# Kernel tuning notes

Measured on AMD Instinct MI355X. Metric: run time of the kernel, lower is better.

Reference implementation:

```python
import jax, jax.numpy as jnp
import numpy as np

D_MODEL = 512
N_HEADS = 8
D_HEAD = D_MODEL // N_HEADS
D_FF = 2048
L_Q = 22          # forecast_horizon
FACTOR = 5        # prob_sparse_factor
EPS = 1e-5


def positional_encoding(L, d):
    pos = jnp.arange(L, dtype=jnp.float32)[:, None]
    div = jnp.exp(-jnp.arange(0, d, 2, dtype=jnp.float32) * (np.log(10000.0) / d))
    pe = jnp.zeros((L, d), dtype=jnp.float32)
    pe = pe.at[:, 0::2].set(jnp.sin(pos * div))
    pe = pe.at[:, 1::2].set(jnp.cos(pos * div))
    return pe


def layernorm(x, g, b):
    mu = x.mean(-1, keepdims=True)
    var = ((x - mu) ** 2).mean(-1, keepdims=True)
    return (x - mu) * jax.lax.rsqrt(var + EPS) * g + b


def setup_inputs() -> dict:
    key = jax.random.key(0)
    ks = jax.random.split(key, 8)
    s = 0.02
    return {
        "encoder_output": jax.random.normal(ks[0], (32, 4096, D_MODEL), dtype=jnp.float32),
        "Wq": jax.random.normal(ks[1], (D_MODEL, D_MODEL), dtype=jnp.float32) * s,
        "bq": jnp.zeros((D_MODEL,), jnp.float32),
        "Wk": jax.random.normal(ks[2], (D_MODEL, D_MODEL), dtype=jnp.float32) * s,
        "bk": jnp.zeros((D_MODEL,), jnp.float32),
        "Wv": jax.random.normal(ks[3], (D_MODEL, D_MODEL), dtype=jnp.float32) * s,
        "bv": jnp.zeros((D_MODEL,), jnp.float32),
        "Wo": jax.random.normal(ks[4], (D_MODEL, D_MODEL), dtype=jnp.float32) * s,
        "bo": jnp.zeros((D_MODEL,), jnp.float32),
        "conv1_w": jax.random.normal(ks[5], (D_FF, D_MODEL), dtype=jnp.float32) * s,  # Conv1d k=1
        "conv1_b": jnp.zeros((D_FF,), jnp.float32),
        "conv2_w": jax.random.normal(ks[6], (D_MODEL, D_FF), dtype=jnp.float32) * s,
        "conv2_b": jnp.zeros((D_MODEL,), jnp.float32),
        "gamma1": jnp.ones((D_MODEL,), jnp.float32),
        "beta1": jnp.zeros((D_MODEL,), jnp.float32),
        "gamma2": jnp.ones((D_MODEL,), jnp.float32),
        "beta2": jnp.zeros((D_MODEL,), jnp.float32),
        "Wout": jax.random.normal(ks[7], (D_MODEL, 1), dtype=jnp.float32) * s,
        "bout": jnp.zeros((1,), jnp.float32),
    }


def reference(encoder_output, Wq, bq, Wk, bk, Wv, bv, Wo, bo,
              conv1_w, conv1_b, conv2_w, conv2_b,
              gamma1, beta1, gamma2, beta2, Wout, bout):
    B, L_K, _ = encoder_output.shape
    # queries are pure positional encodings of a zero dummy input
    pe = positional_encoding(L_Q, D_MODEL)[None]                      # [1, L_Q, d]
    q = (pe @ Wq + bq).reshape(1, L_Q, N_HEADS, D_HEAD).transpose(0, 2, 1, 3)
    k = (encoder_output @ Wk + bk).reshape(B, L_K, N_HEADS, D_HEAD).transpose(0, 2, 1, 3)
    v = (encoder_output @ Wv + bv).reshape(B, L_K, N_HEADS, D_HEAD).transpose(0, 2, 1, 3)

    # --- deterministic ProbSparse query selection (Informer-style) ---
    sample_k = min(L_K, FACTOR * int(np.ceil(np.log(L_K))))           # 45
    n_top = min(L_Q, FACTOR * int(np.ceil(np.log(L_Q))))              # 20
    k_idx = (jnp.arange(sample_k) * L_K) // sample_k                  # deterministic strided key sample
    k_samp = k[:, :, k_idx]                                           # [B,h,sk,dh]
    qk_s = jnp.einsum('ahqd,bhkd->bhqk', q, k_samp)                   # [B,h,L_Q,sk]
    M = qk_s.max(-1) - qk_s.mean(-1)                                  # sparsity measure [B,h,L_Q]
    _, top_idx = jax.lax.top_k(M, n_top)                              # [B,h,n_top]

    q_b = jnp.broadcast_to(q, (B, N_HEADS, L_Q, D_HEAD))
    q_top = jnp.take_along_axis(q_b, top_idx[..., None], axis=2)      # [B,h,n_top,dh]
    scale = 1.0 / np.sqrt(D_HEAD)
    attn = jax.nn.softmax(jnp.einsum('bhud,bhkd->bhuk', q_top, k) * scale, axis=-1)
    ctx_top = jnp.einsum('bhuk,bhkd->bhud', attn, v)                  # [B,h,n_top,dh]

    # non-selected queries get mean(V) (no causal mask: cross attention)
    ctx = jnp.broadcast_to(v.mean(axis=2, keepdims=True), (B, N_HEADS, L_Q, D_HEAD))
    b_i = jnp.arange(B)[:, None, None]
    h_i = jnp.arange(N_HEADS)[None, :, None]
    ctx = ctx.at[b_i, h_i, top_idx].set(ctx_top)

    attn_out = ctx.transpose(0, 2, 1, 3).reshape(B, L_Q, D_MODEL) @ Wo + bo

    # eval-mode dropout is identity -> norm1(attn + dropout(attn)) == norm1(2*attn)
    x = layernorm(attn_out + attn_out, gamma1, beta1)
    ff = jax.nn.relu(x @ conv1_w.T + conv1_b)                          # conv1d k=1 == pointwise linear
    ff = ff @ conv2_w.T + conv2_b
    y = layernorm(x + ff, gamma2, beta2)                               # [B,L_Q,d]
    forecasts = (y @ Wout + bout).squeeze(-1)                          # [B,L_Q]
    return forecasts, y
```

## Files before the change

### kernel.cpp

```cpp
#include <hip/hip_runtime.h>
#include <math.h>

#define B_ 32
#define LK 4096
#define C_ 512
#define H_ 8
#define DH 64
#define U_ 22
#define HU 176
#define HUP 192
#define SK 45
#define NTOP 20
#define DFF 2048
#define EPSF 1e-5f

typedef unsigned short u16;
typedef __attribute__((ext_vector_type(8))) short short8;
typedef __attribute__((ext_vector_type(4))) short short4v;
typedef __attribute__((ext_vector_type(8))) unsigned short ushort8;
typedef __attribute__((ext_vector_type(4))) unsigned short ushort4v;
typedef __attribute__((ext_vector_type(4))) float f32x4;

__device__ __forceinline__ u16 f2b(float f){
  union{float f;unsigned u;} v; v.f=f;
  unsigned r=(v.u + 0x7FFFu + ((v.u>>16)&1u))>>16;
  return (u16)r;
}
__device__ __forceinline__ float b2f(u16 h){
  union{unsigned u;float f;} v; v.u=((unsigned)h)<<16; return v.f;
}
__device__ __forceinline__ short8 ldfrag(const u16* p){
  short4v lo=*(const short4v*)p;
  short4v hi=*(const short4v*)(p+16);
  short8 r;
  r[0]=lo[0];r[1]=lo[1];r[2]=lo[2];r[3]=lo[3];
  r[4]=hi[0];r[5]=hi[1];r[6]=hi[2];r[7]=hi[3];
  return r;
}
__device__ __forceinline__ float blocksum(float v, float* red){
  for(int off=32;off;off>>=1) v+=__shfl_xor(v,off);
  int w=threadIdx.x>>6, lane=threadIdx.x&63;
  if(lane==0) red[w]=v;
  __syncthreads();
  float r=red[0]+red[1]+red[2]+red[3];
  __syncthreads();
  return r;
}

__global__ void k_prep_q(const float* __restrict__ Wq, const float* __restrict__ bq,
                         float* __restrict__ q){
  __shared__ float pe[C_];
  int u=blockIdx.x, t=threadIdx.x;
  float lg = logf(10000.0f)/(float)C_;
  for(int c=t;c<C_;c+=256){
    int i=c>>1;
    float arg=(float)u*expf(-(float)(2*i)*lg);
    pe[c]=(c&1)?cosf(arg):sinf(arg);
  }
  __syncthreads();
  for(int col=t;col<C_;col+=256){
    float acc=0.f;
    for(int c=0;c<C_;c++) acc+=pe[c]*Wq[c*C_+col];
    q[u*C_+col]=acc+bq[col];
  }
}

__global__ void k_qeff(const float* __restrict__ q, const float* __restrict__ Wk,
                       float* __restrict__ qef, u16* __restrict__ qeb){
  int hu=blockIdx.x, t=threadIdx.x;
  int h=hu/U_, u=hu-h*U_;
  __shared__ float qr[DH];
  bool valid=(hu<HU);
  if(t<DH) qr[t]=valid? q[u*C_+h*DH+t] : 0.f;
  __syncthreads();
  for(int c=t;c<C_;c+=256){
    float acc=0.f;
    if(valid){
      const float* wrow=Wk+(size_t)c*C_+h*DH;
      for(int d=0;d<DH;d++) acc+=qr[d]*wrow[d];
    }
    qef[hu*C_+c]=acc;
    qeb[hu*C_+c]=f2b(acc);
  }
}

__global__ void k_sample(const float* __restrict__ enc, const float* __restrict__ qef,
                         unsigned* __restrict__ selmask){
  int bh=blockIdx.x, t=threadIdx.x;
  int b=bh>>3, h=bh&7;
  __shared__ float es[SK][132];
  __shared__ float qe[U_][132];
  __shared__ float qk[U_][SK+3];
  __shared__ float Mv[U_];
  float acc[4]={0.f,0.f,0.f,0.f};
  for(int c0=0;c0<C_;c0+=128){
    __syncthreads();
    for(int i=t;i<SK*128;i+=256){
      int ks=i>>7, c=i&127;
      int row=(ks*LK)/SK;
      es[ks][c]=enc[((size_t)b*LK+row)*C_+c0+c];
    }
    for(int i=t;i<U_*128;i+=256){
      int u=i>>7, c=i&127;
      qe[u][c]=qef[(h*U_+u)*C_+c0+c];
    }
    __syncthreads();
    for(int dd=0;dd<4;dd++){
      int d=t+dd*256;
      if(d<U_*SK){
        int u=d/SK, ks=d-u*SK;
        float s=0.f;
        for(int c=0;c<128;c++) s+=qe[u][c]*es[ks][c];
        acc[dd]+=s;
      }
    }
  }
  for(int dd=0;dd<4;dd++){
    int d=t+dd*256;
    if(d<U_*SK){ int u=d/SK, ks=d-u*SK; qk[u][ks]=acc[dd]; }
  }
  __syncthreads();
  if(t<U_){
    float mx=-1e30f, sm=0.f;
    for(int ks=0;ks<SK;ks++){ float v=qk[t][ks]; mx=fmaxf(mx,v); sm+=v; }
    Mv[t]=mx-sm/(float)SK;
  }
  __syncthreads();
  if(t<64){
    bool sel=false;
    if(t<U_){
      float m=Mv[t]; int rank=0;
      for(int u2=0;u2<U_;u2++){
        float o=Mv[u2];
        if(o>m || (o==m && u2<t)) rank++;
      }
      sel=(rank<NTOP);
    }
    unsigned long long bal=__ballot(sel);
    if(t==0) selmask[bh]=(unsigned)(bal&0x3FFFFFull);
  }
}

__global__ void k_convert(const float* __restrict__ enc, u16* __restrict__ encb,
                          u16* __restrict__ encT){
  int ct=blockIdx.x, lt=blockIdx.y, b=blockIdx.z, t=threadIdx.x;
  __shared__ __align__(16) u16 tile[64][72];
  int l0=lt*64, c0=ct*64;
  for(int p=0;p<4;p++){
    int lr=p*16+(t>>4);
    int cc=(t&15)*4;
    float4 v=*(const float4*)&enc[((size_t)b*LK+l0+lr)*C_+c0+cc];
    u16 h0=f2b(v.x),h1=f2b(v.y),h2=f2b(v.z),h3=f2b(v.w);
    ushort4v o; o[0]=h0;o[1]=h1;o[2]=h2;o[3]=h3;
    *(ushort4v*)&encb[((size_t)b*LK+l0+lr)*C_+c0+cc]=o;
    tile[cc+0][lr]=h0; tile[cc+1][lr]=h1; tile[cc+2][lr]=h2; tile[cc+3][lr]=h3;
  }
  __syncthreads();
  for(int p=0;p<2;p++){
    int cr=p*32+(t>>3), loff=(t&7)*8;
    ushort8 w=*(const ushort8*)&tile[cr][loff];
    *(ushort8*)&encT[((size_t)b*C_+c0+cr)*LK+l0+loff]=w;
  }
}

__global__ void k_colsum(const u16* __restrict__ encT, float* __restrict__ encsum){
  int b=blockIdx.x;
  int w=threadIdx.x>>6, lane=threadIdx.x&63;
  int c=blockIdx.y*4+w;
  const u16* row=encT+((size_t)b*C_+c)*LK;
  float s=0.f;
  for(int i=0;i<8;i++){
    ushort8 v=*(const ushort8*)&row[(i*64+lane)*8];
    for(int j=0;j<8;j++) s+=b2f(v[j]);
  }
  for(int off=32;off;off>>=1) s+=__shfl_down(s,off);
  if(lane==0) encsum[b*C_+c]=s;
}

__global__ __launch_bounds__(256) void k_scores(const u16* __restrict__ encb,
                                                const u16* __restrict__ qeb,
                                                u16* __restrict__ S){
  int nt=blockIdx.x, b=blockIdx.y, t=threadIdx.x;
  __shared__ __align__(16) u16 qa[HUP][40];
  __shared__ __align__(16) u16 et[128][40];
  int l0=nt*128;
  int w=t>>6, lane=t&63;
  int arow=lane&15, kgrp=(lane>>4)*4;
  f32x4 acc[12][2];
  #pragma unroll
  for(int i=0;i<12;i++){
    acc[i][0]=(f32x4){0.f,0.f,0.f,0.f};
    acc[i][1]=(f32x4){0.f,0.f,0.f,0.f};
  }
  for(int kc=0;kc<C_;kc+=32){
    __syncthreads();
    for(int i=t;i<768;i+=256){
      int r=i>>2, off=(i&3)*8;
      *(ushort8*)&qa[r][off]=*(const ushort8*)&qeb[(size_t)r*C_+kc+off];
    }
    for(int i=t;i<512;i+=256){
      int l=i>>2, off=(i&3)*8;
      *(ushort8*)&et[l][off]=*(const ushort8*)&encb[((size_t)b*LK+l0+l)*C_+kc+off];
    }
    __syncthreads();
    short8 bf0=ldfrag(&et[w*32+arow][kgrp]);
    short8 bf1=ldfrag(&et[w*32+16+arow][kgrp]);
    #pragma unroll
    for(int m=0;m<12;m++){
      short8 af=ldfrag(&qa[m*16+arow][kgrp]);
      acc[m][0]=__builtin_amdgcn_mfma_f32_16x16x32_bf16(af,bf0,acc[m][0],0,0,0);
      acc[m][1]=__builtin_amdgcn_mfma_f32_16x16x32_bf16(af,bf1,acc[m][1],0,0,0);
    }
  }
  int dcol=lane&15, drow=(lane>>4)*4;
  #pragma unroll
  for(int m=0;m<12;m++)
    #pragma unroll
    for(int ns=0;ns<2;ns++){
      size_t base=((size_t)b*HUP+m*16+drow)*LK + l0 + w*32 + ns*16 + dcol;
      #pragma unroll
      for(int r=0;r<4;r++)
        S[base+(size_t)r*LK]=f2b(acc[m][ns][r]);
    }
}

__global__ void k_softmax(u16* __restrict__ S){
  int hu=blockIdx.x, b=blockIdx.y, t=threadIdx.x;
  u16* row=S+((size_t)b*HUP+hu)*LK;
  __shared__ float red[8];
  __shared__ float red2[8];
  float v[16];
  ushort8 r0=*(const ushort8*)&row[t*16];
  ushort8 r1=*(const ushort8*)&row[t*16+8];
  #pragma unroll
  for(int j=0;j<8;j++){ v[j]=b2f(r0[j]); v[8+j]=b2f(r1[j]); }
  float mx=-1e30f;
  #pragma unroll
  for(int j=0;j<16;j++) mx=fmaxf(mx,v[j]);
  for(int off=32;off;off>>=1) mx=fmaxf(mx,__shfl_xor(mx,off));
  int w=t>>6, lane=t&63;
  if(lane==0) red[w]=mx;
  __syncthreads();
  mx=fmaxf(fmaxf(red[0],red[1]),fmaxf(red[2],red[3]));
  const float scale=0.125f;
  float sm=0.f;
  #pragma unroll
  for(int j=0;j<16;j++){ v[j]=__expf((v[j]-mx)*scale); sm+=v[j]; }
  for(int off=32;off;off>>=1) sm+=__shfl_xor(sm,off);
  if(lane==0) red2[w]=sm;
  __syncthreads();
  sm=red2[0]+red2[1]+red2[2]+red2[3];
  float inv=1.f/sm;
  ushort8 o0,o1;
  #pragma unroll
  for(int j=0;j<8;j++){ o0[j]=f2b(v[j]*inv); o1[j]=f2b(v[8+j]*inv); }
  *(ushort8*)&row[t*16]=o0;
  *(ushort8*)&row[t*16+8]=o1;
}

__global__ __launch_bounds__(256) void k_pv(const u16* __restrict__ S,
                                            const u16* __restrict__ encT,
                                            float* __restrict__ ctxA){
  int f=blockIdx.x, t=threadIdx.x;
  int xcd=f&7, s=f>>3;
  int mt=s&3, g=(s>>2)*8+xcd;
  int nt=g>>7, bz=g&127;
  int b=bz>>2, kch=bz&3;
  __shared__ __align__(16) u16 pa[48][72];
  __shared__ __align__(16) u16 et[128][72];
  int hu0=mt*48, c0=nt*128;
  int w=t>>6, lane=t&63;
  int arow=lane&15, kgrp=(lane>>4)*4;
  f32x4 acc[3][2];
  #pragma unroll
  for(int i=0;i<3;i++)
    #pragma unroll
    for(int j=0;j<2;j++) acc[i][j]=(f32x4){0.f,0.f,0.f,0.f};
  int lbase=kch*1024;
  for(int l0=lbase;l0<lbase+1024;l0+=64){
    __syncthreads();
    for(int i=t;i<384;i+=256){
      int r=i>>3, off=(i&7)*8;
      *(ushort8*)&pa[r][off]=*(const ushort8*)&S[((size_t)b*HUP+hu0+r)*LK+l0+off];
    }
    for(int i=t;i<1024;i+=256){
      int r=i>>3, off=(i&7)*8;
      *(ushort8*)&et[r][off]=*(const ushort8*)&encT[((size_t)b*C_+c0+r)*LK+l0+off];
    }
    __syncthreads();
    #pragma unroll
    for(int ks=0;ks<2;ks++){
      short8 af0=ldfrag(&pa[arow][ks*32+kgrp]);
      short8 af1=ldfrag(&pa[16+arow][ks*32+kgrp]);
      short8 af2=ldfrag(&pa[32+arow][ks*32+kgrp]);
      #pragma unroll
      for(int ns=0;ns<2;ns++){
        short8 bf=ldfrag(&et[w*32+ns*16+arow][ks*32+kgrp]);
        acc[0][ns]=__builtin_amdgcn_mfma_f32_16x16x32_bf16(af0,bf,acc[0][ns],0,0,0);
        acc[1][ns]=__builtin_amdgcn_mfma_f32_16x16x32_bf16(af1,bf,acc[1][ns],0,0,0);
        acc[2][ns]=__builtin_amdgcn_mfma_f32_16x16x32_bf16(af2,bf,acc[2][ns],0,0,0);
      }
    }
  }
  int dcol=lane&15, drow=(lane>>4)*4;
  #pragma unroll
  for(int m=0;m<3;m++)
    #pragma unroll
    for(int ns=0;ns<2;ns++)
      #pragma unroll
      for(int r=0;r<4;r++){
        int hu=hu0+m*16+drow+r, c=c0+w*32+ns*16+dcol;
        atomicAdd(&ctxA[((size_t)b*HUP+hu)*C_+c],acc[m][ns][r]);
      }
}

__global__ void k_ctxproj(const float* __restrict__ ctxA, const float* __restrict__ encsum,
                          const unsigned* __restrict__ selmask, const float* __restrict__ Wv,
                          const float* __restrict__ bv, float* __restrict__ ctx){
  int u=blockIdx.x, b=blockIdx.y, t=threadIdx.x;
  __shared__ float R[H_][C_];
  for(int h=0;h<H_;h++){
    bool sel=(selmask[b*H_+h]>>u)&1u;
    const float* src=sel? &ctxA[((size_t)b*HUP+h*U_+u)*C_] : &encsum[b*C_];
    float sc=sel? 1.f : (1.f/(float)LK);
    for(int c=t;c<C_;c+=256) R[h][c]=src[c]*sc;
  }
  __syncthreads();
  for(int hd=t;hd<C_;hd+=256){
    int h=hd>>6;
    float a=0.f;
    for(int c=0;c<C_;c++) a+=R[h][c]*Wv[(size_t)c*C_+hd];
    ctx[((size_t)(b*U_+u))*C_+hd]=a+bv[hd];
  }
}

__global__ void k_wo_ln1(const float* __restrict__ ctx, const float* __restrict__ Wo,
                         const float* __restrict__ bo, const float* __restrict__ g1,
                         const float* __restrict__ be1, float* __restrict__ x,
                         u16* __restrict__ xb){
  int u=blockIdx.x, b=blockIdx.y, t=threadIdx.x;
  __shared__ float row[C_];
  __shared__ float red[8];
  size_t r0=(size_t)(b*U_+u)*C_;
  for(int c=t;c<C_;c+=256) row[c]=ctx[r0+c];
  __syncthreads();
  float a0=0.f,a1=0.f;
  for(int c=0;c<C_;c++){
    float rv=row[c];
    a0+=rv*Wo[(size_t)c*C_+t];
    a1+=rv*Wo[(size_t)c*C_+t+256];
  }
  a0=2.f*(a0+bo[t]); a1=2.f*(a1+bo[t+256]);
  float mu=blocksum(a0+a1,red)*(1.f/(float)C_);
  float d0=a0-mu, d1=a1-mu;
  float var=blocksum(d0*d0+d1*d1,red)*(1.f/(float)C_);
  float rs=rsqrtf(var+EPSF);
  float x0=d0*rs*g1[t]+be1[t];
  float x1=d1*rs*g1[t+256]+be1[t+256];
  x[r0+t]=x0;
  x[r0+t+256]=x1;
  xb[r0+t]=f2b(x0);
  xb[r0+t+256]=f2b(x1);
}

__global__ void k_convw(const float* __restrict__ W1, const float* __restrict__ W2,
                        u16* __restrict__ W1b, u16* __restrict__ W2b){
  size_t i=((size_t)blockIdx.x*256+threadIdx.x)*8;
  const float* src; u16* dst;
  const size_t NW=(size_t)DFF*C_;
  if(i<NW){ src=W1; dst=W1b; } else { src=W2; dst=W2b; i-=NW; }
  float4 a=*(const float4*)&src[i];
  float4 b=*(const float4*)&src[i+4];
  ushort8 o;
  o[0]=f2b(a.x);o[1]=f2b(a.y);o[2]=f2b(a.z);o[3]=f2b(a.w);
  o[4]=f2b(b.x);o[5]=f2b(b.y);o[6]=f2b(b.z);o[7]=f2b(b.w);
  *(ushort8*)&dst[i]=o;
}

__global__ __launch_bounds__(256) void k_ff1m(const u16* __restrict__ xb,
                                              const u16* __restrict__ W1b,
                                              const float* __restrict__ b1,
                                              u16* __restrict__ ff1b){
  int mt=blockIdx.x, ntb=blockIdx.y, t=threadIdx.x;
  __shared__ __align__(16) u16 a_lds[32][520];
  __shared__ __align__(16) u16 et[256][40];
  int m0=mt*32, n0=ntb*256;
  for(int i=t;i<32*64;i+=256){
    int r=i>>6, cc=(i&63)*8;
    *(ushort8*)&a_lds[r][cc]=*(const ushort8*)&xb[(size_t)(m0+r)*C_+cc];
  }
  int w=t>>6, lane=t&63;
  int arow=lane&15, kgrp=(lane>>4)*4;
  f32x4 acc[2][4];
  #pragma unroll
  for(int i=0;i<2;i++)
    #pragma unroll
    for(int j=0;j<4;j++) acc[i][j]=(f32x4){0.f,0.f,0.f,0.f};
  for(int kc=0;kc<C_;kc+=32){
    __syncthreads();
    for(int i=t;i<1024;i+=256){
      int n=i>>2, off=(i&3)*8;
      *(ushort8*)&et[n][off]=*(const ushort8*)&W1b[(size_t)(n0+n)*C_+kc+off];
    }
    __syncthreads();
    short8 af0=ldfrag(&a_lds[arow][kc+kgrp]);
    short8 af1=ldfrag(&a_lds[16+arow][kc+kgrp]);
    #pragma unroll
    for(int ns=0;ns<4;ns++){
      short8 bf=ldfrag(&et[w*64+ns*16+arow][kgrp]);
      acc[0][ns]=__builtin_amdgcn_mfma_f32_16x16x32_bf16(af0,bf,acc[0][ns],0,0,0);
      acc[1][ns]=__builtin_amdgcn_mfma_f32_16x16x32_bf16(af1,bf,acc[1][ns],0,0,0);
    }
  }
  int dcol=lane&15, drow=(lane>>4)*4;
  #pragma unroll
  for(int ms=0;ms<2;ms++)
    #pragma unroll
    for(int ns=0;ns<4;ns++){
      int n=n0+w*64+ns*16+dcol;
      float bb=b1[n];
      #pragma unroll
      for(int r=0;r<4;r++){
        int m=m0+ms*16+drow+r;
        float v=acc[ms][ns][r]+bb;
        ff1b[(size_t)m*DFF+n]=f2b(v>0.f?v:0.f);
      }
    }
}

__global__ __launch_bounds__(256) void k_ff2m(const u16* __restrict__ ff1b,
                                              const u16* __restrict__ W2b,
                                              float* __restrict__ out){
  int mt=blockIdx.x, ntb=blockIdx.y, kch=blockIdx.z, t=threadIdx.x;
  __shared__ __align__(16) u16 a_lds[32][520];
  __shared__ __align__(16) u16 et[256][40];
  int m0=mt*32, n0=ntb*256, k0=kch*512;
  for(int i=t;i<32*64;i+=256){
    int r=i>>6, cc=(i&63)*8;
    *(ushort8*)&a_lds[r][cc]=*(const ushort8*)&ff1b[(size_t)(m0+r)*DFF+k0+cc];
  }
  int w=t>>6, lane=t&63;
  int arow=lane&15, kgrp=(lane>>4)*4;
  f32x4 acc[2][4];
  #pragma unroll
  for(int i=0;i<2;i++)
    #pragma unroll
    for(int j=0;j<4;j++) acc[i][j]=(f32x4){0.f,0.f,0.f,0.f};
  for(int kc=0;kc<512;kc+=32){
    __syncthreads();
    for(int i=t;i<1024;i+=256){
      int n=i>>2, off=(i&3)*8;
      *(ushort8*)&et[n][off]=*(const ushort8*)&W2b[(size_t)(n0+n)*DFF+k0+kc+off];
    }
    __syncthreads();
    short8 af0=ldfrag(&a_lds[arow][kc+kgrp]);
    short8 af1=ldfrag(&a_lds[16+arow][kc+kgrp]);
    #pragma unroll
    for(int ns=0;ns<4;ns++){
      short8 bf=ldfrag(&et[w*64+ns*16+arow][kgrp]);
      acc[0][ns]=__builtin_amdgcn_mfma_f32_16x16x32_bf16(af0,bf,acc[0][ns],0,0,0);
      acc[1][ns]=__builtin_amdgcn_mfma_f32_16x16x32_bf16(af1,bf,acc[1][ns],0,0,0);
    }
  }
  int dcol=lane&15, drow=(lane>>4)*4;
  #pragma unroll
  for(int ms=0;ms<2;ms++)
    #pragma unroll
    for(int ns=0;ns<4;ns++){
      int n=n0+w*64+ns*16+dcol;
      #pragma unroll
      for(int r=0;r<4;r++){
        int m=m0+ms*16+drow+r;
        atomicAdd(&out[(size_t)m*C_+n],acc[ms][ns][r]);
      }
    }
}

__global__ void k_ln2(const float* __restrict__ x, const float* __restrict__ ff2,
                      const float* __restrict__ b2, const float* __restrict__ g2,
                      const float* __restrict__ be2, const float* __restrict__ Wout,
                      const float* __restrict__ bout, float* __restrict__ dout){
  int u=blockIdx.x, b=blockIdx.y, t=threadIdx.x;
  __shared__ float red[8];
  size_t r0=(size_t)(b*U_+u)*C_;
  float s0=x[r0+t]+ff2[r0+t]+b2[t];
  float s1=x[r0+t+256]+ff2[r0+t+256]+b2[t+256];
  float mu=blocksum(s0+s1,red)*(1.f/(float)C_);
  float d0=s0-mu, d1=s1-mu;
  float var=blocksum(d0*d0+d1*d1,red)*(1.f/(float)C_);
  float rs=rsqrtf(var+EPSF);
  float y0=d0*rs*g2[t]+be2[t];
  float y1=d1*rs*g2[t+256]+be2[t+256];
  float* Y=dout+B_*U_;
  Y[r0+t]=y0;
  Y[r0+t+256]=y1;
  float f=blocksum(y0*Wout[t]+y1*Wout[t+256],red);
  if(t==0) dout[b*U_+u]=f+bout[0];
}

extern "C" void kernel_launch(void* const* d_in, const int* in_sizes, int n_in,
                              void* d_out, int out_size, void* d_ws, size_t ws_size,
                              hipStream_t stream){
  (void)in_sizes;(void)n_in;(void)out_size;(void)ws_size;
  const float* enc =(const float*)d_in[0];
  const float* Wq  =(const float*)d_in[1];
  const float* bq  =(const float*)d_in[2];
  const float* Wk  =(const float*)d_in[3];
  const float* Wv  =(const float*)d_in[5];
  const float* bv  =(const float*)d_in[6];
  const float* Wo  =(const float*)d_in[7];
  const float* bo  =(const float*)d_in[8];
  const float* W1  =(const float*)d_in[9];
  const float* b1  =(const float*)d_in[10];
  const float* W2  =(const float*)d_in[11];
  const float* b2  =(const float*)d_in[12];
  const float* g1  =(const float*)d_in[13];
  const float* be1 =(const float*)d_in[14];
  const float* g2  =(const float*)d_in[15];
  const float* be2 =(const float*)d_in[16];
  const float* Wout=(const float*)d_in[17];
  const float* bout=(const float*)d_in[18];

  char* ws=(char*)d_ws;
  float*    q      =(float*)   (ws+0);
  float*    qef    =(float*)   (ws+45056);
  u16*      qeb    =(u16*)     (ws+438272);
  unsigned* selmask=(unsigned*)(ws+634880);
  float*    encsum =(float*)   (ws+635904);
  u16*      encb   =(u16*)     (ws+701440);
  u16*      encT   =(u16*)     (ws+134919168);
  u16*      S      =(u16*)     (ws+269136896);
  float*    ctxA   =(float*)   (ws+701440);
  float*    ctx    =(float*)   (ws+13284352);
  float*    x      =(float*)   (ws+14726144);
  u16*      ff1b   =(u16*)     (ws+16167936);
  float*    ff2    =(float*)   (ws+21935104);
  u16*      W1b    =(u16*)     (ws+23376896);
  u16*      W2b    =(u16*)     (ws+25474048);
  u16*      xb     =(u16*)     (ws+27571200);

  hipLaunchKernelGGL(k_prep_q, dim3(22),      dim3(256),0,stream, Wq,bq,q);
  hipLaunchKernelGGL(k_qeff,   dim3(192),     dim3(256),0,stream, q,Wk,qef,qeb);
  hipLaunchKernelGGL(k_sample, dim3(256),     dim3(256),0,stream, enc,qef,selmask);
  hipLaunchKernelGGL(k_convert,dim3(8,64,32), dim3(256),0,stream, enc,encb,encT);
  hipLaunchKernelGGL(k_colsum, dim3(32,128),  dim3(256),0,stream, encT,encsum);
  hipLaunchKernelGGL(k_scores, dim3(32,32),   dim3(256),0,stream, encb,qeb,S);
  hipLaunchKernelGGL(k_softmax,dim3(192,32),  dim3(256),0,stream, S);
  hipMemsetAsync(ctxA,0,12582912,stream);
  hipLaunchKernelGGL(k_pv,     dim3(2048),    dim3(256),0,stream, S,encT,ctxA);
  hipLaunchKernelGGL(k_ctxproj,dim3(22,32),   dim3(256),0,stream, ctxA,encsum,selmask,Wv,bv,ctx);
  hipLaunchKernelGGL(k_convw,  dim3(1024),    dim3(256),0,stream, W1,W2,W1b,W2b);
  hipLaunchKernelGGL(k_wo_ln1, dim3(22,32),   dim3(256),0,stream, ctx,Wo,bo,g1,be1,x,xb);
  hipLaunchKernelGGL(k_ff1m,   dim3(22,8),    dim3(256),0,stream, xb,W1b,b1,ff1b);
  hipMemsetAsync(ff2,0,1441792,stream);
  hipLaunchKernelGGL(k_ff2m,   dim3(22,2,4),  dim3(256),0,stream, ff1b,W2b,ff2);
  hipLaunchKernelGGL(k_ln2,    dim3(22,32),   dim3(256),0,stream, x,ff2,b2,g2,be2,Wout,bout,(float*)d_out);
}
```

Baseline: 924.8 us.

## Fuse column sum into convert and retile PV to cover all query rows per block

The column sum of the encoder is now computed inside the conversion kernel from its shared-memory tile and accumulated with atomics into a zeroed buffer. This removes a separate kernel that reread the whole transposed encoder. The PV kernel now uses 512-thread blocks that each hold all 192 query rows, so every encoder tile is loaded once per batch and column chunk instead of once per query row group. The cost is more accumulator registers per thread, split-K over 8 chunks, and the extra atomics this adds.

```diff
diff --git a/kernel.cpp b/kernel.cpp
--- a/kernel.cpp
+++ b/kernel.cpp
@@ -142,7 +142,7 @@
 }
 
 __global__ void k_convert(const float* __restrict__ enc, u16* __restrict__ encb,
-                          u16* __restrict__ encT){
+                          u16* __restrict__ encT, float* __restrict__ encsum){
   int ct=blockIdx.x, lt=blockIdx.y, b=blockIdx.z, t=threadIdx.x;
   __shared__ __align__(16) u16 tile[64][72];
   int l0=lt*64, c0=ct*64;
@@ -161,20 +161,13 @@
     ushort8 w=*(const ushort8*)&tile[cr][loff];
     *(ushort8*)&encT[((size_t)b*C_+c0+cr)*LK+l0+loff]=w;
   }
-}
-
-__global__ void k_colsum(const u16* __restrict__ encT, float* __restrict__ encsum){
-  int b=blockIdx.x;
-  int w=threadIdx.x>>6, lane=threadIdx.x&63;
-  int c=blockIdx.y*4+w;
-  const u16* row=encT+((size_t)b*C_+c)*LK;
+  int cr=t>>2, qq=t&3;
   float s=0.f;
-  for(int i=0;i<8;i++){
-    ushort8 v=*(const ushort8*)&row[(i*64+lane)*8];
-    for(int j=0;j<8;j++) s+=b2f(v[j]);
-  }
-  for(int off=32;off;off>>=1) s+=__shfl_down(s,off);
-  if(lane==0) encsum[b*C_+c]=s;
+  #pragma unroll
+  for(int j=0;j<16;j++) s+=b2f(tile[cr][qq*16+j]);
+  s+=__shfl_xor(s,1);
+  s+=__shfl_xor(s,2);
+  if(qq==0) atomicAdd(&encsum[b*C_+c0+cr],s);
 }
 
 __global__ __launch_bounds__(256) void k_scores(const u16* __restrict__ encb,
@@ -258,60 +251,49 @@
   *(ushort8*)&row[t*16+8]=o1;
 }
 
-__global__ __launch_bounds__(256) void k_pv(const u16* __restrict__ S,
+__global__ __launch_bounds__(512) void k_pv(const u16* __restrict__ S,
                                             const u16* __restrict__ encT,
                                             float* __restrict__ ctxA){
-  int f=blockIdx.x, t=threadIdx.x;
-  int xcd=f&7, s=f>>3;
-  int mt=s&3, g=(s>>2)*8+xcd;
-  int nt=g>>7, bz=g&127;
-  int b=bz>>2, kch=bz&3;
-  __shared__ __align__(16) u16 pa[48][72];
+  int nt=blockIdx.x, b=blockIdx.y, kch=blockIdx.z, t=threadIdx.x;
+  __shared__ __align__(16) u16 pa[HUP][72];
   __shared__ __align__(16) u16 et[128][72];
-  int hu0=mt*48, c0=nt*128;
-  int w=t>>6, lane=t&63;
+  int c0=nt*128;
+  int wv=t>>6, lane=t&63;
   int arow=lane&15, kgrp=(lane>>4)*4;
-  f32x4 acc[3][2];
-  #pragma unroll
-  for(int i=0;i<3;i++)
-    #pragma unroll
-    for(int j=0;j<2;j++) acc[i][j]=(f32x4){0.f,0.f,0.f,0.f};
-  int lbase=kch*1024;
-  for(int l0=lbase;l0<lbase+1024;l0+=64){
-    __syncthreads();
-    for(int i=t;i<384;i+=256){
+  f32x4 acc[12];
+  #pragma unroll
+  for(int i=0;i<12;i++) acc[i]=(f32x4){0.f,0.f,0.f,0.f};
+  int lbase=kch*512;
+  for(int l0=lbase;l0<lbase+512;l0+=64){
+    __syncthreads();
+    for(int i=t;i<1536;i+=512){
       int r=i>>3, off=(i&7)*8;
-      *(ushort8*)&pa[r][off]=*(const ushort8*)&S[((size_t)b*HUP+hu0+r)*LK+l0+off];
-    }
-    for(int i=t;i<1024;i+=256){
+      *(ushort8*)&pa[r][off]=*(const ushort8*)&S[((size_t)b*HUP+r)*LK+l0+off];
+    }
+    for(int i=t;i<1024;i+=512){
       int r=i>>3, off=(i&7)*8;
       *(ushort8*)&et[r][off]=*(const ushort8*)&encT[((size_t)b*C_+c0+r)*LK+l0+off];
     }
     __syncthreads();
     #pragma unroll
     for(int ks=0;ks<2;ks++){
-      short8 af0=ldfrag(&pa[arow][ks*32+kgrp]);
-      short8 af1=ldfrag(&pa[16+arow][ks*32+kgrp]);
-      short8 af2=ldfrag(&pa[32+arow][ks*32+kgrp]);
+      short8 bf=ldfrag(&et[wv*16+arow][ks*32+kgrp]);
       #pragma unroll
-      for(int ns=0;ns<2;ns++){
-        short8 bf=ldfrag(&et[w*32+ns*16+arow][ks*32+kgrp]);
-        acc[0][ns]=__builtin_amdgcn_mfma_f32_16x16x32_bf16(af0,bf,acc[0][ns],0,0,0);
-        acc[1][ns]=__builtin_amdgcn_mfma_f32_16x16x32_bf16(af1,bf,acc[1][ns],0,0,0);
-        acc[2][ns]=__builtin_amdgcn_mfma_f32_16x16x32_bf16(af2,bf,acc[2][ns],0,0,0);
+      for(int m=0;m<12;m++){
+        short8 af=ldfrag(&pa[m*16+arow][ks*32+kgrp]);
+        acc[m]=__builtin_amdgcn_mfma_f32_16x16x32_bf16(af,bf,acc[m],0,0,0);
       }
     }
   }
   int dcol=lane&15, drow=(lane>>4)*4;
-  #pragma unroll
-  for(int m=0;m<3;m++)
-    #pragma unroll
-    for(int ns=0;ns<2;ns++)
-      #pragma unroll
-      for(int r=0;r<4;r++){
-        int hu=hu0+m*16+drow+r, c=c0+w*32+ns*16+dcol;
-        atomicAdd(&ctxA[((size_t)b*HUP+hu)*C_+c],acc[m][ns][r]);
-      }
+  int c=c0+wv*16+dcol;
+  #pragma unroll
+  for(int m=0;m<12;m++)
+    #pragma unroll
+    for(int r=0;r<4;r++){
+      int hu=m*16+drow+r;
+      atomicAdd(&ctxA[((size_t)b*HUP+hu)*C_+c],acc[m][r]);
+    }
 }
 
 __global__ void k_ctxproj(const float* __restrict__ ctxA, const float* __restrict__ encsum,
@@ -542,12 +524,12 @@
   hipLaunchKernelGGL(k_prep_q, dim3(22),      dim3(256),0,stream, Wq,bq,q);
   hipLaunchKernelGGL(k_qeff,   dim3(192),     dim3(256),0,stream, q,Wk,qef,qeb);
   hipLaunchKernelGGL(k_sample, dim3(256),     dim3(256),0,stream, enc,qef,selmask);
-  hipLaunchKernelGGL(k_convert,dim3(8,64,32), dim3(256),0,stream, enc,encb,encT);
-  hipLaunchKernelGGL(k_colsum, dim3(32,128),  dim3(256),0,stream, encT,encsum);
+  hipMemsetAsync(encsum,0,65536,stream);
+  hipLaunchKernelGGL(k_convert,dim3(8,64,32), dim3(256),0,stream, enc,encb,encT,encsum);
   hipLaunchKernelGGL(k_scores, dim3(32,32),   dim3(256),0,stream, encb,qeb,S);
   hipLaunchKernelGGL(k_softmax,dim3(192,32),  dim3(256),0,stream, S);
   hipMemsetAsync(ctxA,0,12582912,stream);
-  hipLaunchKernelGGL(k_pv,     dim3(2048),    dim3(256),0,stream, S,encT,ctxA);
+  hipLaunchKernelGGL(k_pv,     dim3(4,32,8),  dim3(512),0,stream, S,encT,ctxA);
   hipLaunchKernelGGL(k_ctxproj,dim3(22,32),   dim3(256),0,stream, ctxA,encsum,selmask,Wv,bv,ctx);
   hipLaunchKernelGGL(k_convw,  dim3(1024),    dim3(256),0,stream, W1,W2,W1b,W2b);
   hipLaunchKernelGGL(k_wo_ln1, dim3(22,32),   dim3(256),0,stream, ctx,Wo,bo,g1,be1,x,xb);
```

After: 895.5 us. -3.2%, faster.
